# Kernel optimization log

Hardware: AMD Instinct MI355X
Metric: run time of the kernel (lower is better)

Reference implementation:

```python
import jax, jax.numpy as jnp
import numpy as np

N = 100000   # nodes
E = 500000   # edges per relation
R = 3        # relations (etypes)
L = 2        # layers
F = 300      # input features
H = 256      # hidden
C = 23       # classes


def setup_inputs() -> dict:
    key = jax.random.key(0)
    ks = jax.random.split(key, 12)
    s = 0.05
    return {
        "x": jax.random.normal(ks[0], (N, F), jnp.float32),
        "edge_src": jax.random.randint(ks[1], (R, E), 0, N, dtype=jnp.int32),
        "edge_dst": jax.random.randint(ks[2], (R, E), 0, N, dtype=jnp.int32),
        "W_feat": jax.random.normal(ks[3], (F, H), jnp.float32) * s,
        "b_feat": jnp.zeros((H,), jnp.float32),
        "g_feat": jnp.ones((H,), jnp.float32),
        "beta_feat": jnp.zeros((H,), jnp.float32),
        "gcn_W": jax.random.normal(ks[4], (L, R, H, H), jnp.float32) * s,
        "gcn_b": jnp.zeros((L, R, H), jnp.float32),
        "skip_W": jax.random.normal(ks[5], (L, H, H), jnp.float32) * s,
        "skip_b": jnp.zeros((L, H), jnp.float32),
        "bn_g": jnp.ones((L, H), jnp.float32),
        "bn_b": jnp.zeros((L, H), jnp.float32),
        "W_c1": jax.random.normal(ks[6], (H, H), jnp.float32) * s,
        "b_c1": jnp.zeros((H,), jnp.float32),
        "g_c": jnp.ones((H,), jnp.float32),
        "beta_c": jnp.zeros((H,), jnp.float32),
        "W_c2": jax.random.normal(ks[7], (H, C), jnp.float32) * s,
        "b_c2": jnp.zeros((C,), jnp.float32),
    }


def _bn(h, g, b):
    # BatchNorm1d, training-mode batch stats (biased var), eps=1e-5
    m = h.mean(0)
    v = jnp.mean((h - m) ** 2, 0)
    return g * (h - m) * jax.lax.rsqrt(v + 1e-5) + b


def _het_forward(x, edge_src, edge_dst, W_feat, b_feat, g_feat, beta_feat,
                 gcn_W, gcn_b, skip_W, skip_b, bn_g, bn_b,
                 W_c1, b_c1, g_c, beta_c, W_c2, b_c2):
    seg = jax.ops.segment_sum
    ones = jnp.ones((E,), jnp.float32)
    # feat_reduce: Linear + BN + ReLU
    h = jax.nn.relu(_bn(x @ W_feat + b_feat, g_feat, beta_feat))  # [N, H]
    for l in range(L):
        h_res = h @ skip_W[l] + skip_b[l]
        rel = []
        for r in range(R):  # per-relation GraphConv (DGL norm='both')
            src, dst = edge_src[r], edge_dst[r]
            dout = jnp.clip(seg(ones, src, num_segments=N), 1.0, None)
            din = jnp.clip(seg(ones, dst, num_segments=N), 1.0, None)
            xs = h * jax.lax.rsqrt(dout)[:, None]          # src-normalize
            m = seg(xs[src], dst, num_segments=N)          # gather-scatter
            m = m * jax.lax.rsqrt(din)[:, None]            # dst-normalize
            rel.append(m @ gcn_W[l, r] + gcn_b[l, r])
        h = jnp.mean(jnp.stack(rel, 0), 0)  # het_combine='mean'
        h = h + h_res
        h = jax.nn.leaky_relu(_bn(h, bn_g[l], bn_b[l]), 0.01)
        # dropout is identity in eval mode
    # classification head
    h = jax.nn.relu(_bn(h @ W_c1 + b_c1, g_c, beta_c))
    return h @ W_c2 + b_c2  # [N, C]


def reference(x, edge_src, edge_dst, W_feat, b_feat, g_feat, beta_feat,
              gcn_W, gcn_b, skip_W, skip_b, bn_g, bn_b,
              W_c1, b_c1, g_c, beta_c, W_c2, b_c2):
    return _het_forward(x, edge_src, edge_dst, W_feat, b_feat, g_feat,
                        beta_feat, gcn_W, gcn_b, skip_W, skip_b, bn_g, bn_b,
                        W_c1, b_c1, g_c, beta_c, W_c2, b_c2)
```

## Files before the change

### kernel.cpp

```cpp
#include <hip/hip_runtime.h>

#define NN 100000
#define EE 500000
#define RR 3
#define LL 2
#define FF 300
#define HH 256
#define CC 23
#define MPAD 100096
#define SCHUNK 2048
#define SNB ((NN + SCHUNK - 1) / SCHUNK)

static inline int cdiv_h(int a, int b) { return (a + b - 1) / b; }

typedef __attribute__((ext_vector_type(8))) short bf16x8;
typedef __attribute__((ext_vector_type(4))) float f32x4;

__device__ inline unsigned short f2bf(float f) {
    union { float f; unsigned int u; } v; v.f = f;
    unsigned int r = v.u + 0x7fff + ((v.u >> 16) & 1);
    return (unsigned short)(r >> 16);
}
__device__ inline float bf2f(unsigned short u) {
    union { unsigned int u; float f; } v; v.u = ((unsigned int)u) << 16;
    return v.f;
}
__device__ inline void gl_lds16(const void* g, void* l) {
    __builtin_amdgcn_global_load_lds((const __attribute__((address_space(1))) unsigned int*)g,
                                     (__attribute__((address_space(3))) unsigned int*)l,
                                     16, 0, 0);
}

__global__ void hist_kernel(const int* __restrict__ src, const int* __restrict__ dst,
                            int* __restrict__ cnt_out, int* __restrict__ cnt_in,
                            int RE, int Eper) {
    int i = blockIdx.x * blockDim.x + threadIdx.x;
    if (i >= RE) return;
    int r = i / Eper;
    atomicAdd(&cnt_out[r * NN + src[i]], 1);
    atomicAdd(&cnt_in[r * NN + dst[i]], 1);
}

__global__ void rs_kernel(const int* __restrict__ cnt_out, const int* __restrict__ cnt_in,
                          float* __restrict__ rs_out, float* __restrict__ rs_in, int total) {
    int i = blockIdx.x * blockDim.x + threadIdx.x;
    if (i >= total) return;
    rs_out[i] = rsqrtf(fmaxf((float)cnt_out[i], 1.0f));
    rs_in[i]  = rsqrtf(fmaxf((float)cnt_in[i], 1.0f));
}

__global__ __launch_bounds__(256) void scan_a(const int* __restrict__ cnt, int* __restrict__ bsum) {
    int r = blockIdx.y, b = blockIdx.x, t = threadIdx.x;
    const int* c = cnt + (size_t)r * NN;
    int base = b * SCHUNK;
    int s = 0;
    for (int i = t; i < SCHUNK; i += 256) {
        int idx = base + i;
        if (idx < NN) s += c[idx];
    }
#pragma unroll
    for (int o = 1; o < 64; o <<= 1) s += __shfl_xor(s, o);
    __shared__ int sh[4];
    if ((t & 63) == 0) sh[t >> 6] = s;
    __syncthreads();
    if (t == 0) bsum[r * SNB + b] = sh[0] + sh[1] + sh[2] + sh[3];
}

__global__ void scan_b(int* __restrict__ bsum, int* __restrict__ offs) {
    int r = threadIdx.x;
    if (r >= RR) return;
    int* bs = bsum + r * SNB;
    int run = 0;
    for (int i = 0; i < SNB; i++) { int v = bs[i]; bs[i] = run; run += v; }
    offs[(size_t)r * (NN + 1) + NN] = run;
}

__global__ __launch_bounds__(256) void scan_c(const int* __restrict__ cnt, const int* __restrict__ bsum,
                                              int* __restrict__ offs, int* __restrict__ cur) {
    int r = blockIdx.y, b = blockIdx.x, t = threadIdx.x;
    const int* c = cnt + (size_t)r * NN;
    int base = b * SCHUNK + t * 8;
    int v[8]; int s = 0;
#pragma unroll
    for (int j = 0; j < 8; j++) {
        int idx = base + j;
        v[j] = (idx < NN) ? c[idx] : 0;
        s += v[j];
    }
    __shared__ int sh[256];
    sh[t] = s;
    __syncthreads();
    for (int d = 1; d < 256; d <<= 1) {
        int x = (t >= d) ? sh[t - d] : 0;
        __syncthreads();
        sh[t] += x;
        __syncthreads();
    }
    int run = sh[t] - s + bsum[r * SNB + b];
    int* orow = offs + (size_t)r * (NN + 1);
    int* crow = cur + (size_t)r * NN;
#pragma unroll
    for (int j = 0; j < 8; j++) {
        int idx = base + j;
        if (idx < NN) { orow[idx] = run; crow[idx] = run; }
        run += v[j];
    }
}

__global__ void fill_kernel(const int* __restrict__ src, const int* __restrict__ dst,
                            const float* __restrict__ rs_out,
                            int* __restrict__ cur, int2* __restrict__ srcw,
                            int RE, int Eper) {
    int i = blockIdx.x * blockDim.x + threadIdx.x;
    if (i >= RE) return;
    int r = i / Eper;
    int d = dst[i];
    int s = src[i];
    float w = rs_out[r * NN + s];
    int pos = atomicAdd(&cur[r * NN + d], 1);
    srcw[(size_t)r * Eper + pos] = make_int2(s, __float_as_int(w));
}

__global__ void convert_x(const float* __restrict__ x, unsigned short* __restrict__ xpad) {
    int row = blockIdx.x;
    int col = threadIdx.x;
    float v = (row < NN && col < FF) ? x[(size_t)row * FF + col] : 0.f;
    xpad[(size_t)row * 320 + col] = f2bf(v);
}

__global__ void wprep_feat(const float* __restrict__ W, unsigned short* __restrict__ Bt) {
    int n = blockIdx.x;
    int k = threadIdx.x;
    float v = (k < FF) ? W[(size_t)k * HH + n] : 0.f;
    Bt[(size_t)n * 320 + k] = f2bf(v);
}

__global__ void wprep_layer(const float* __restrict__ skipW, const float* __restrict__ gcnW,
                            unsigned short* __restrict__ Bt) {
    int idx = blockIdx.x * blockDim.x + threadIdx.x;
    int n = idx >> 10, k = idx & 1023;
    int seg = k >> 8, k2 = k & 255;
    float v = (seg == 0) ? skipW[(size_t)k2 * HH + n]
                         : gcnW[(size_t)(seg - 1) * HH * HH + (size_t)k2 * HH + n] * (1.0f / 3.0f);
    Bt[(size_t)n * 1024 + k] = f2bf(v);
}

__global__ void bias_layer(const float* __restrict__ skip_b, const float* __restrict__ gcn_b,
                           float* __restrict__ bias) {
    int t = threadIdx.x;
    bias[t] = skip_b[t] + (gcn_b[t] + gcn_b[HH + t] + gcn_b[2 * HH + t]) * (1.0f / 3.0f);
}

__global__ void wprep_c1(const float* __restrict__ W, unsigned short* __restrict__ Bt) {
    int idx = blockIdx.x * blockDim.x + threadIdx.x;
    int n = idx >> 8, k = idx & 255;
    Bt[(size_t)n * HH + k] = f2bf(W[(size_t)k * HH + n]);
}

__global__ void wprep_c2(const float* __restrict__ W, unsigned short* __restrict__ Bt) {
    int n = blockIdx.x;
    int k = threadIdx.x;
    float v = (n < CC) ? W[(size_t)k * CC + n] : 0.f;
    Bt[(size_t)n * HH + k] = f2bf(v);
}

__global__ __launch_bounds__(256) void agg_bf16(unsigned short* __restrict__ hcat,
                                                const int* __restrict__ offs_all,
                                                const int2* __restrict__ srcw_all,
                                                const float* __restrict__ rs_in_all) {
    int r = blockIdx.y;
    const int* offs = offs_all + (size_t)r * (NN + 1);
    const int2* srcw = srcw_all + (size_t)r * EE;
    const float* rs_i = rs_in_all + (size_t)r * NN;
    int wave = threadIdx.x >> 6;
    int lane = threadIdx.x & 63;
    int node = blockIdx.x * 4 + wave;
    if (node >= NN) return;
    int s0 = __builtin_amdgcn_readfirstlane(offs[node]);
    int s1 = __builtin_amdgcn_readfirstlane(offs[node + 1]);
    int cnt = s1 - s0;
    const int2* ew = srcw + s0;
    const unsigned short* hb = hcat + lane * 4;
    float a0 = 0.f, a1 = 0.f, a2 = 0.f, a3 = 0.f;
    int k = 0;
    for (; k + 8 <= cnt; k += 8) {
        int2 e[8];
#pragma unroll
        for (int q = 0; q < 8; q++) e[q] = ew[k + q];
        ushort4 hv[8];
#pragma unroll
        for (int q = 0; q < 8; q++) hv[q] = *(const ushort4*)(hb + (size_t)e[q].x * 1024);
#pragma unroll
        for (int q = 0; q < 8; q++) {
            float u = __int_as_float(e[q].y);
            a0 += u * bf2f(hv[q].x); a1 += u * bf2f(hv[q].y);
            a2 += u * bf2f(hv[q].z); a3 += u * bf2f(hv[q].w);
        }
    }
    if (k + 4 <= cnt) {
        int2 e[4];
#pragma unroll
        for (int q = 0; q < 4; q++) e[q] = ew[k + q];
        ushort4 hv[4];
#pragma unroll
        for (int q = 0; q < 4; q++) hv[q] = *(const ushort4*)(hb + (size_t)e[q].x * 1024);
#pragma unroll
        for (int q = 0; q < 4; q++) {
            float u = __int_as_float(e[q].y);
            a0 += u * bf2f(hv[q].x); a1 += u * bf2f(hv[q].y);
            a2 += u * bf2f(hv[q].z); a3 += u * bf2f(hv[q].w);
        }
        k += 4;
    }
    int rem = cnt - k;
    if (rem > 0) {
        int2 e[3];
#pragma unroll
        for (int q = 0; q < 3; q++) {
            int kk = k + q; if (kk > cnt - 1) kk = cnt - 1;
            e[q] = ew[kk];
        }
        ushort4 hv[3];
#pragma unroll
        for (int q = 0; q < 3; q++) hv[q] = *(const ushort4*)(hb + (size_t)e[q].x * 1024);
        float u0 = __int_as_float(e[0].y);
        float u1 = rem > 1 ? __int_as_float(e[1].y) : 0.f;
        float u2 = rem > 2 ? __int_as_float(e[2].y) : 0.f;
        a0 += u0 * bf2f(hv[0].x) + u1 * bf2f(hv[1].x) + u2 * bf2f(hv[2].x);
        a1 += u0 * bf2f(hv[0].y) + u1 * bf2f(hv[1].y) + u2 * bf2f(hv[2].y);
        a2 += u0 * bf2f(hv[0].z) + u1 * bf2f(hv[1].z) + u2 * bf2f(hv[2].z);
        a3 += u0 * bf2f(hv[0].w) + u1 * bf2f(hv[1].w) + u2 * bf2f(hv[2].w);
    }
    float wi = rs_i[node];
    ushort4 o;
    o.x = f2bf(a0 * wi); o.y = f2bf(a1 * wi);
    o.z = f2bf(a2 * wi); o.w = f2bf(a3 * wi);
    *(ushort4*)(hcat + (size_t)node * 1024 + 256 * (r + 1) + lane * 4) = o;
}

__global__ __launch_bounds__(256) void mfma_gemm(const unsigned short* __restrict__ A, int ldA,
                                                 const unsigned short* __restrict__ Bt,
                                                 const float* __restrict__ bias,
                                                 void* __restrict__ Cv, int ldC,
                                                 int Nstore, int K, int c_bf16,
                                                 float* __restrict__ stats) {
    __shared__ unsigned short ldsA[2][128 * 32];
    __shared__ unsigned short ldsB[2][128 * 32];
    int tid = threadIdx.x;
    int w = tid >> 6, lane = tid & 63;
    int quad = lane >> 4, lr = lane & 15;
    int bm = blockIdx.y * 128, bn = blockIdx.x * 128;
    int wm = w >> 1, wn = w & 1;
    int lrow = lane >> 2;
    int lslot = lane & 3;

    f32x4 acc[4][4];
#pragma unroll
    for (int i = 0; i < 4; i++)
#pragma unroll
        for (int j = 0; j < 4; j++) acc[i][j] = (f32x4){0.f, 0.f, 0.f, 0.f};

    for (int k0 = 0; k0 < K; k0 += 64) {
#pragma unroll
        for (int h = 0; h < 2; h++) {
            int kk0 = k0 + h * 32;
#pragma unroll
            for (int c = 0; c < 2; c++) {
                int cc = w * 2 + c;
                int rA = cc * 16 + lrow;
                int cg = lslot ^ ((rA >> 1) & 3);
                gl_lds16(A + (size_t)(bm + rA) * ldA + kk0 + cg * 8, &ldsA[h][cc * 512]);
                gl_lds16(Bt + (size_t)(bn + rA) * K + kk0 + cg * 8, &ldsB[h][cc * 512]);
            }
        }
        __syncthreads();
#pragma unroll
        for (int h = 0; h < 2; h++) {
            bf16x8 af[4], bfr[4];
#pragma unroll
            for (int i = 0; i < 4; i++) {
                int r = wm * 64 + i * 16 + lr;
                int s = quad ^ ((r >> 1) & 3);
                af[i] = *(const bf16x8*)&ldsA[h][r * 32 + s * 8];
            }
#pragma unroll
            for (int j = 0; j < 4; j++) {
                int n = wn * 64 + j * 16 + lr;
                int s = quad ^ ((n >> 1) & 3);
                bfr[j] = *(const bf16x8*)&ldsB[h][n * 32 + s * 8];
            }
#pragma unroll
            for (int i = 0; i < 4; i++)
#pragma unroll
                for (int j = 0; j < 4; j++)
                    acc[i][j] = __builtin_amdgcn_mfma_f32_16x16x32_bf16(af[i], bfr[j], acc[i][j], 0, 0, 0);
        }
        __syncthreads();
    }

    float* Cf = (float*)Cv;
    unsigned short* Cb = (unsigned short*)Cv;
#pragma unroll
    for (int j = 0; j < 4; j++) {
        int col = bn + wn * 64 + j * 16 + lr;
        if (col >= Nstore) continue;
        float bv = bias ? bias[col] : 0.f;
        float ssum = 0.f, ssq = 0.f;
#pragma unroll
        for (int i = 0; i < 4; i++) {
#pragma unroll
            for (int v = 0; v < 4; v++) {
                int row = bm + wm * 64 + i * 16 + quad * 4 + v;
                if (row < NN) {
                    float val = acc[i][j][v] + bv;
                    if (c_bf16) Cb[(size_t)row * ldC + col] = f2bf(val);
                    else        Cf[(size_t)row * ldC + col] = val;
                    ssum += val; ssq += val * val;
                }
            }
        }
        if (stats) {
            ssum += __shfl_xor(ssum, 16); ssum += __shfl_xor(ssum, 32);
            ssq  += __shfl_xor(ssq, 16);  ssq  += __shfl_xor(ssq, 32);
            if (quad == 0) {
                atomicAdd(&stats[col], ssum);
                atomicAdd(&stats[HH + col], ssq);
            }
        }
    }
}

__global__ void bn_coef(const float* __restrict__ stats, const float* __restrict__ g,
                        const float* __restrict__ b, float* __restrict__ coef, float invM) {
    int c = threadIdx.x;
    float mean = stats[c] * invM;
    float var = stats[HH + c] * invM - mean * mean;
    float inv = rsqrtf(var + 1e-5f);
    float sc = g[c] * inv;
    coef[c] = sc;
    coef[HH + c] = b[c] - mean * sc;
}

__global__ __launch_bounds__(256) void bn_apply_v(const unsigned short* __restrict__ Z,
                                                  const float* __restrict__ coef,
                                                  unsigned short* __restrict__ out, int act) {
    int idx = blockIdx.x * blockDim.x + threadIdx.x;
    if (idx >= NN * 32) return;
    int row = idx >> 5, cg = (idx & 31) * 8;
    union { uint4 u; unsigned short s[8]; } zin, zo;
    zin.u = *(const uint4*)(Z + (size_t)row * HH + cg);
    f32x4 sc0 = *(const f32x4*)(coef + cg);
    f32x4 sc1 = *(const f32x4*)(coef + cg + 4);
    f32x4 sh0 = *(const f32x4*)(coef + HH + cg);
    f32x4 sh1 = *(const f32x4*)(coef + HH + cg + 4);
#pragma unroll
    for (int j = 0; j < 8; j++) {
        float sc = (j < 4) ? sc0[j] : sc1[j - 4];
        float sh = (j < 4) ? sh0[j] : sh1[j - 4];
        float v = bf2f(zin.s[j]) * sc + sh;
        if (act == 1) v = fmaxf(v, 0.f);
        else v = (v < 0.f) ? 0.01f * v : v;
        zo.s[j] = f2bf(v);
    }
    *(uint4*)(out + (size_t)row * 1024 + cg) = zo.u;
}

extern "C" void kernel_launch(void* const* d_in, const int* in_sizes, int n_in,
                              void* d_out, int out_size, void* d_ws, size_t ws_size,
                              hipStream_t stream) {
    const float* x        = (const float*)d_in[0];
    const int*   esrc     = (const int*)d_in[1];
    const int*   edst     = (const int*)d_in[2];
    const float* W_feat   = (const float*)d_in[3];
    const float* b_feat   = (const float*)d_in[4];
    const float* g_feat   = (const float*)d_in[5];
    const float* beta_feat= (const float*)d_in[6];
    const float* gcn_W    = (const float*)d_in[7];
    const float* gcn_b    = (const float*)d_in[8];
    const float* skip_W   = (const float*)d_in[9];
    const float* skip_b   = (const float*)d_in[10];
    const float* bn_g     = (const float*)d_in[11];
    const float* bn_b     = (const float*)d_in[12];
    const float* W_c1     = (const float*)d_in[13];
    const float* b_c1     = (const float*)d_in[14];
    const float* g_c      = (const float*)d_in[15];
    const float* beta_c   = (const float*)d_in[16];
    const float* W_c2     = (const float*)d_in[17];
    const float* b_c2     = (const float*)d_in[18];
    float* out = (float*)d_out;
    (void)in_sizes; (void)n_in; (void)out_size; (void)ws_size;

    char* w = (char*)d_ws;
    size_t off = 0;
    auto alloc = [&](size_t bytes) { void* p = w + off; off += (bytes + 255) & ~(size_t)255; return p; };
    unsigned short* hcat = (unsigned short*)alloc((size_t)MPAD * 1024 * 2);
    unsigned short* xpad = hcat;
    unsigned short* c_acc = (unsigned short*)alloc((size_t)NN * HH * 2);
    float* f_stats = (float*)alloc(4 * 2 * HH * 4);
    float* f_coef  = (float*)alloc(2 * HH * 4);
    float* f_rs_out = (float*)alloc((size_t)RR * NN * 4);
    float* f_rs_in  = (float*)alloc((size_t)RR * NN * 4);
    int* i_cnt_out = (int*)alloc((size_t)RR * NN * 4);
    int* i_cnt_in  = (int*)alloc((size_t)RR * NN * 4);
    int* i_off     = (int*)alloc((size_t)RR * (NN + 1) * 4);
    int* i_cur     = (int*)alloc((size_t)RR * NN * 4);
    int2* i_srcw   = (int2*)alloc((size_t)RR * EE * 8);
    int* i_bsum    = (int*)alloc((size_t)RR * SNB * 4);
    unsigned short* Bt_feat = (unsigned short*)alloc(256 * 320 * 2);
    unsigned short* Bt_l0   = (unsigned short*)alloc(256 * 1024 * 2);
    unsigned short* Bt_l1   = (unsigned short*)alloc(256 * 1024 * 2);
    unsigned short* Bt_c1   = (unsigned short*)alloc(256 * 256 * 2);
    unsigned short* Bt_c2   = (unsigned short*)alloc(128 * 256 * 2);
    float* bias_l0 = (float*)alloc(HH * 4);
    float* bias_l1 = (float*)alloc(HH * 4);

    const float invM = 1.0f / (float)NN;
    const int RE = RR * EE;

    (void)hipMemsetAsync(i_cnt_out, 0, (size_t)RR * NN * 4, stream);
    (void)hipMemsetAsync(i_cnt_in, 0, (size_t)RR * NN * 4, stream);
    (void)hipMemsetAsync(f_stats, 0, 4 * 2 * HH * 4, stream);
    hist_kernel<<<cdiv_h(RE, 256), 256, 0, stream>>>(esrc, edst, i_cnt_out, i_cnt_in, RE, EE);
    rs_kernel<<<cdiv_h(RR * NN, 256), 256, 0, stream>>>(i_cnt_out, i_cnt_in, f_rs_out, f_rs_in, RR * NN);
    scan_a<<<dim3(SNB, RR), 256, 0, stream>>>(i_cnt_in, i_bsum);
    scan_b<<<1, 64, 0, stream>>>(i_bsum, i_off);
    scan_c<<<dim3(SNB, RR), 256, 0, stream>>>(i_cnt_in, i_bsum, i_off, i_cur);
    fill_kernel<<<cdiv_h(RE, 256), 256, 0, stream>>>(esrc, edst, f_rs_out, i_cur, i_srcw, RE, EE);

    convert_x<<<MPAD, 320, 0, stream>>>(x, xpad);
    wprep_feat<<<256, 320, 0, stream>>>(W_feat, Bt_feat);
    wprep_layer<<<1024, 256, 0, stream>>>(skip_W, gcn_W, Bt_l0);
    wprep_layer<<<1024, 256, 0, stream>>>(skip_W + (size_t)HH * HH, gcn_W + (size_t)RR * HH * HH, Bt_l1);
    bias_layer<<<1, 256, 0, stream>>>(skip_b, gcn_b, bias_l0);
    bias_layer<<<1, 256, 0, stream>>>(skip_b + HH, gcn_b + (size_t)RR * HH, bias_l1);
    wprep_c1<<<256, 256, 0, stream>>>(W_c1, Bt_c1);
    wprep_c2<<<128, 256, 0, stream>>>(W_c2, Bt_c2);

    dim3 grid_H(2, MPAD / 128);
    dim3 grid_C(1, MPAD / 128);
    const int nblk_a = cdiv_h(NN * 32, 256);
    float* st0 = f_stats;
    float* st1 = f_stats + 2 * HH;
    float* st2 = f_stats + 4 * HH;
    float* st3 = f_stats + 6 * HH;

    mfma_gemm<<<grid_H, 256, 0, stream>>>(xpad, 320, Bt_feat, b_feat, c_acc, HH, HH, 320, 1, st0);
    bn_coef<<<1, 256, 0, stream>>>(st0, g_feat, beta_feat, f_coef, invM);
    bn_apply_v<<<nblk_a, 256, 0, stream>>>(c_acc, f_coef, hcat, 1);

    for (int l = 0; l < LL; l++) {
        agg_bf16<<<dim3(cdiv_h(NN, 4), RR), 256, 0, stream>>>(hcat, i_off, i_srcw, f_rs_in);
        float* st = l ? st2 : st1;
        mfma_gemm<<<grid_H, 256, 0, stream>>>(hcat, 1024, l ? Bt_l1 : Bt_l0,
                                              l ? bias_l1 : bias_l0, c_acc, HH, HH, 1024, 1, st);
        bn_coef<<<1, 256, 0, stream>>>(st, bn_g + (size_t)l * HH, bn_b + (size_t)l * HH, f_coef, invM);
        bn_apply_v<<<nblk_a, 256, 0, stream>>>(c_acc, f_coef, hcat, 2);
    }

    mfma_gemm<<<grid_H, 256, 0, stream>>>(hcat, 1024, Bt_c1, b_c1, c_acc, HH, HH, 256, 1, st3);
    bn_coef<<<1, 256, 0, stream>>>(st3, g_c, beta_c, f_coef, invM);
    bn_apply_v<<<nblk_a, 256, 0, stream>>>(c_acc, f_coef, hcat + 256, 1);
    mfma_gemm<<<grid_C, 256, 0, stream>>>(hcat + 256, 1024, Bt_c2, b_c2, out, CC, CC, 256, 0, nullptr);
}
```

Baseline: 1.233 ms.

## Widen GEMM tile to full N, merge weight-prep and BN-coef launches

The GEMM now uses a 128x256 tile per block covering all 256 output columns, so each A tile is read once rather than twice, with launch bounds set to 2 waves per SIMD. The seven weight-prep and bias kernels become a single launch, and BN coefficient computation moves into each bn_apply block through shared memory, dropping separate one-block launches. The wider tile doubles accumulators and B LDS, which may cut occupancy. The final 23-column GEMM now computes a full 256-wide tile with padded Bt_c2, adding wasted work there.

```diff
diff --git a/kernel.cpp b/kernel.cpp
--- a/kernel.cpp
+++ b/kernel.cpp
@@ -128,40 +128,44 @@
     xpad[(size_t)row * 320 + col] = f2bf(v);
 }
 
-__global__ void wprep_feat(const float* __restrict__ W, unsigned short* __restrict__ Bt) {
-    int n = blockIdx.x;
-    int k = threadIdx.x;
-    float v = (k < FF) ? W[(size_t)k * HH + n] : 0.f;
-    Bt[(size_t)n * 320 + k] = f2bf(v);
-}
-
-__global__ void wprep_layer(const float* __restrict__ skipW, const float* __restrict__ gcnW,
-                            unsigned short* __restrict__ Bt) {
-    int idx = blockIdx.x * blockDim.x + threadIdx.x;
-    int n = idx >> 10, k = idx & 1023;
-    int seg = k >> 8, k2 = k & 255;
-    float v = (seg == 0) ? skipW[(size_t)k2 * HH + n]
-                         : gcnW[(size_t)(seg - 1) * HH * HH + (size_t)k2 * HH + n] * (1.0f / 3.0f);
-    Bt[(size_t)n * 1024 + k] = f2bf(v);
-}
-
-__global__ void bias_layer(const float* __restrict__ skip_b, const float* __restrict__ gcn_b,
-                           float* __restrict__ bias) {
-    int t = threadIdx.x;
-    bias[t] = skip_b[t] + (gcn_b[t] + gcn_b[HH + t] + gcn_b[2 * HH + t]) * (1.0f / 3.0f);
-}
-
-__global__ void wprep_c1(const float* __restrict__ W, unsigned short* __restrict__ Bt) {
-    int idx = blockIdx.x * blockDim.x + threadIdx.x;
-    int n = idx >> 8, k = idx & 255;
-    Bt[(size_t)n * HH + k] = f2bf(W[(size_t)k * HH + n]);
-}
-
-__global__ void wprep_c2(const float* __restrict__ W, unsigned short* __restrict__ Bt) {
-    int n = blockIdx.x;
-    int k = threadIdx.x;
-    float v = (n < CC) ? W[(size_t)k * CC + n] : 0.f;
-    Bt[(size_t)n * HH + k] = f2bf(v);
+__global__ void prep_weights(const float* __restrict__ W_feat,
+                             const float* __restrict__ skip_W, const float* __restrict__ gcn_W,
+                             const float* __restrict__ skip_b, const float* __restrict__ gcn_b,
+                             const float* __restrict__ W_c1, const float* __restrict__ W_c2,
+                             unsigned short* __restrict__ Bt_feat,
+                             unsigned short* __restrict__ Bt_l0, unsigned short* __restrict__ Bt_l1,
+                             unsigned short* __restrict__ Bt_c1, unsigned short* __restrict__ Bt_c2,
+                             float* __restrict__ bias_l0, float* __restrict__ bias_l1) {
+    int b = blockIdx.x, t = threadIdx.x;
+    if (b < 256) {
+        for (int k = t; k < 320; k += 256) {
+            float v = (k < FF) ? W_feat[(size_t)k * HH + b] : 0.f;
+            Bt_feat[(size_t)b * 320 + k] = f2bf(v);
+        }
+    } else if (b < 2304) {
+        int l = (b < 1280) ? 0 : 1;
+        unsigned short* Bt = l ? Bt_l1 : Bt_l0;
+        const float* sW = skip_W + (size_t)l * HH * HH;
+        const float* gW = gcn_W + (size_t)l * RR * HH * HH;
+        int idx = (b - (l ? 1280 : 256)) * 256 + t;
+        int n = idx >> 10, k = idx & 1023;
+        int seg = k >> 8, k2 = k & 255;
+        float v = (seg == 0) ? sW[(size_t)k2 * HH + n]
+                             : gW[(size_t)(seg - 1) * HH * HH + (size_t)k2 * HH + n] * (1.0f / 3.0f);
+        Bt[(size_t)n * 1024 + k] = f2bf(v);
+    } else if (b < 2560) {
+        int idx = (b - 2304) * 256 + t;
+        int n = idx >> 8, k = idx & 255;
+        Bt_c1[(size_t)n * HH + k] = f2bf(W_c1[(size_t)k * HH + n]);
+    } else if (b < 2816) {
+        int n = b - 2560, k = t;
+        float v = (n < CC) ? W_c2[(size_t)k * CC + n] : 0.f;
+        Bt_c2[(size_t)n * HH + k] = f2bf(v);
+    } else {
+        bias_l0[t] = skip_b[t] + (gcn_b[t] + gcn_b[HH + t] + gcn_b[2 * HH + t]) * (1.0f / 3.0f);
+        bias_l1[t] = skip_b[HH + t] +
+                     (gcn_b[RR * HH + t] + gcn_b[(RR + 1) * HH + t] + gcn_b[(RR + 2) * HH + t]) * (1.0f / 3.0f);
+    }
 }
 
 __global__ __launch_bounds__(256) void agg_bf16(unsigned short* __restrict__ hcat,
@@ -238,25 +242,24 @@
     *(ushort4*)(hcat + (size_t)node * 1024 + 256 * (r + 1) + lane * 4) = o;
 }
 
-__global__ __launch_bounds__(256) void mfma_gemm(const unsigned short* __restrict__ A, int ldA,
-                                                 const unsigned short* __restrict__ Bt,
-                                                 const float* __restrict__ bias,
-                                                 void* __restrict__ Cv, int ldC,
-                                                 int Nstore, int K, int c_bf16,
-                                                 float* __restrict__ stats) {
+__global__ __launch_bounds__(256, 2) void mfma_gemm(const unsigned short* __restrict__ A, int ldA,
+                                                    const unsigned short* __restrict__ Bt,
+                                                    const float* __restrict__ bias,
+                                                    void* __restrict__ Cv, int ldC,
+                                                    int Nstore, int K, int c_bf16,
+                                                    float* __restrict__ stats) {
     __shared__ unsigned short ldsA[2][128 * 32];
-    __shared__ unsigned short ldsB[2][128 * 32];
+    __shared__ unsigned short ldsB[2][256 * 32];
     int tid = threadIdx.x;
     int w = tid >> 6, lane = tid & 63;
     int quad = lane >> 4, lr = lane & 15;
-    int bm = blockIdx.y * 128, bn = blockIdx.x * 128;
-    int wm = w >> 1, wn = w & 1;
+    int bm = blockIdx.x * 128;
     int lrow = lane >> 2;
     int lslot = lane & 3;
 
-    f32x4 acc[4][4];
-#pragma unroll
-    for (int i = 0; i < 4; i++)
+    f32x4 acc[8][4];
+#pragma unroll
+    for (int i = 0; i < 8; i++)
 #pragma unroll
         for (int j = 0; j < 4; j++) acc[i][j] = (f32x4){0.f, 0.f, 0.f, 0.f};
 
@@ -270,27 +273,33 @@
                 int rA = cc * 16 + lrow;
                 int cg = lslot ^ ((rA >> 1) & 3);
                 gl_lds16(A + (size_t)(bm + rA) * ldA + kk0 + cg * 8, &ldsA[h][cc * 512]);
-                gl_lds16(Bt + (size_t)(bn + rA) * K + kk0 + cg * 8, &ldsB[h][cc * 512]);
+            }
+#pragma unroll
+            for (int c = 0; c < 4; c++) {
+                int cc = w * 4 + c;
+                int rB = cc * 16 + lrow;
+                int cg = lslot ^ ((rB >> 1) & 3);
+                gl_lds16(Bt + (size_t)rB * K + kk0 + cg * 8, &ldsB[h][cc * 512]);
             }
         }
         __syncthreads();
 #pragma unroll
         for (int h = 0; h < 2; h++) {
-            bf16x8 af[4], bfr[4];
-#pragma unroll
-            for (int i = 0; i < 4; i++) {
-                int r = wm * 64 + i * 16 + lr;
+            bf16x8 af[8], bfr[4];
+#pragma unroll
+            for (int i = 0; i < 8; i++) {
+                int r = i * 16 + lr;
                 int s = quad ^ ((r >> 1) & 3);
                 af[i] = *(const bf16x8*)&ldsA[h][r * 32 + s * 8];
             }
 #pragma unroll
             for (int j = 0; j < 4; j++) {
-                int n = wn * 64 + j * 16 + lr;
+                int n = w * 64 + j * 16 + lr;
                 int s = quad ^ ((n >> 1) & 3);
                 bfr[j] = *(const bf16x8*)&ldsB[h][n * 32 + s * 8];
             }
 #pragma unroll
-            for (int i = 0; i < 4; i++)
+            for (int i = 0; i < 8; i++)
 #pragma unroll
                 for (int j = 0; j < 4; j++)
                     acc[i][j] = __builtin_amdgcn_mfma_f32_16x16x32_bf16(af[i], bfr[j], acc[i][j], 0, 0, 0);
@@ -302,15 +311,15 @@
     unsigned short* Cb = (unsigned short*)Cv;
 #pragma unroll
     for (int j = 0; j < 4; j++) {
-        int col = bn + wn * 64 + j * 16 + lr;
+        int col = w * 64 + j * 16 + lr;
         if (col >= Nstore) continue;
         float bv = bias ? bias[col] : 0.f;
         float ssum = 0.f, ssq = 0.f;
 #pragma unroll
-        for (int i = 0; i < 4; i++) {
+        for (int i = 0; i < 8; i++) {
 #pragma unroll
             for (int v = 0; v < 4; v++) {
-                int row = bm + wm * 64 + i * 16 + quad * 4 + v;
+                int row = bm + i * 16 + quad * 4 + v;
                 if (row < NN) {
                     float val = acc[i][j][v] + bv;
                     if (c_bf16) Cb[(size_t)row * ldC + col] = f2bf(val);
@@ -330,34 +339,30 @@
     }
 }
 
-__global__ void bn_coef(const float* __restrict__ stats, const float* __restrict__ g,
-                        const float* __restrict__ b, float* __restrict__ coef, float invM) {
-    int c = threadIdx.x;
-    float mean = stats[c] * invM;
-    float var = stats[HH + c] * invM - mean * mean;
-    float inv = rsqrtf(var + 1e-5f);
-    float sc = g[c] * inv;
-    coef[c] = sc;
-    coef[HH + c] = b[c] - mean * sc;
-}
-
 __global__ __launch_bounds__(256) void bn_apply_v(const unsigned short* __restrict__ Z,
-                                                  const float* __restrict__ coef,
+                                                  const float* __restrict__ stats,
+                                                  const float* __restrict__ g,
+                                                  const float* __restrict__ b,
                                                   unsigned short* __restrict__ out, int act) {
-    int idx = blockIdx.x * blockDim.x + threadIdx.x;
+    __shared__ float sc_s[HH], sh_s[HH];
+    int t = threadIdx.x;
+    {
+        float mean = stats[t] * (1.0f / NN);
+        float var = stats[HH + t] * (1.0f / NN) - mean * mean;
+        float inv = rsqrtf(var + 1e-5f);
+        float sc = g[t] * inv;
+        sc_s[t] = sc;
+        sh_s[t] = b[t] - mean * sc;
+    }
+    __syncthreads();
+    int idx = blockIdx.x * 256 + t;
     if (idx >= NN * 32) return;
     int row = idx >> 5, cg = (idx & 31) * 8;
     union { uint4 u; unsigned short s[8]; } zin, zo;
     zin.u = *(const uint4*)(Z + (size_t)row * HH + cg);
-    f32x4 sc0 = *(const f32x4*)(coef + cg);
-    f32x4 sc1 = *(const f32x4*)(coef + cg + 4);
-    f32x4 sh0 = *(const f32x4*)(coef + HH + cg);
-    f32x4 sh1 = *(const f32x4*)(coef + HH + cg + 4);
 #pragma unroll
     for (int j = 0; j < 8; j++) {
-        float sc = (j < 4) ? sc0[j] : sc1[j - 4];
-        float sh = (j < 4) ? sh0[j] : sh1[j - 4];
-        float v = bf2f(zin.s[j]) * sc + sh;
+        float v = bf2f(zin.s[j]) * sc_s[cg + j] + sh_s[cg + j];
         if (act == 1) v = fmaxf(v, 0.f);
         else v = (v < 0.f) ? 0.01f * v : v;
         zo.s[j] = f2bf(v);
@@ -397,7 +402,6 @@
     unsigned short* xpad = hcat;
     unsigned short* c_acc = (unsigned short*)alloc((size_t)NN * HH * 2);
     float* f_stats = (float*)alloc(4 * 2 * HH * 4);
-    float* f_coef  = (float*)alloc(2 * HH * 4);
     float* f_rs_out = (float*)alloc((size_t)RR * NN * 4);
     float* f_rs_in  = (float*)alloc((size_t)RR * NN * 4);
     int* i_cnt_out = (int*)alloc((size_t)RR * NN * 4);
@@ -410,11 +414,10 @@
     unsigned short* Bt_l0   = (unsigned short*)alloc(256 * 1024 * 2);
     unsigned short* Bt_l1   = (unsigned short*)alloc(256 * 1024 * 2);
     unsigned short* Bt_c1   = (unsigned short*)alloc(256 * 256 * 2);
-    unsigned short* Bt_c2   = (unsigned short*)alloc(128 * 256 * 2);
+    unsigned short* Bt_c2   = (unsigned short*)alloc(256 * 256 * 2);
     float* bias_l0 = (float*)alloc(HH * 4);
     float* bias_l1 = (float*)alloc(HH * 4);
 
-    const float invM = 1.0f / (float)NN;
     const int RE = RR * EE;
 
     (void)hipMemsetAsync(i_cnt_out, 0, (size_t)RR * NN * 4, stream);
@@ -428,37 +431,29 @@
     fill_kernel<<<cdiv_h(RE, 256), 256, 0, stream>>>(esrc, edst, f_rs_out, i_cur, i_srcw, RE, EE);
 
     convert_x<<<MPAD, 320, 0, stream>>>(x, xpad);
-    wprep_feat<<<256, 320, 0, stream>>>(W_feat, Bt_feat);
-    wprep_layer<<<1024, 256, 0, stream>>>(skip_W, gcn_W, Bt_l0);
-    wprep_layer<<<1024, 256, 0, stream>>>(skip_W + (size_t)HH * HH, gcn_W + (size_t)RR * HH * HH, Bt_l1);
-    bias_layer<<<1, 256, 0, stream>>>(skip_b, gcn_b, bias_l0);
-    bias_layer<<<1, 256, 0, stream>>>(skip_b + HH, gcn_b + (size_t)RR * HH, bias_l1);
-    wprep_c1<<<256, 256, 0, stream>>>(W_c1, Bt_c1);
-    wprep_c2<<<128, 256, 0, stream>>>(W_c2, Bt_c2);
-
-    dim3 grid_H(2, MPAD / 128);
-    dim3 grid_C(1, MPAD / 128);
-    const int nblk_a = cdiv_h(NN * 32, 256);
+    prep_weights<<<2817, 256, 0, stream>>>(W_feat, skip_W, gcn_W, skip_b, gcn_b, W_c1, W_c2,
+                                           Bt_feat, Bt_l0, Bt_l1, Bt_c1, Bt_c2, bias_l0, bias_l1);
+
+    const int grid_M = MPAD / 128;
+    const int nblk_a = NN * 32 / 256;
     float* st0 = f_stats;
     float* st1 = f_stats + 2 * HH;
     float* st2 = f_stats + 4 * HH;
     float* st3 = f_stats + 6 * HH;
 
-    mfma_gemm<<<grid_H, 256, 0, stream>>>(xpad, 320, Bt_feat, b_feat, c_acc, HH, HH, 320, 1, st0);
-    bn_coef<<<1, 256, 0, stream>>>(st0, g_feat, beta_feat, f_coef, invM);
-    bn_apply_v<<<nblk_a, 256, 0, stream>>>(c_acc, f_coef, hcat, 1);
+    mfma_gemm<<<grid_M, 256, 0, stream>>>(xpad, 320, Bt_feat, b_feat, c_acc, HH, HH, 320, 1, st0);
+    bn_apply_v<<<nblk_a, 256, 0, stream>>>(c_acc, st0, g_feat, beta_feat, hcat, 1);
 
     for (int l = 0; l < LL; l++) {
         agg_bf16<<<dim3(cdiv_h(NN, 4), RR), 256, 0, stream>>>(hcat, i_off, i_srcw, f_rs_in);
         float* st = l ? st2 : st1;
-        mfma_gemm<<<grid_H, 256, 0, stream>>>(hcat, 1024, l ? Bt_l1 : Bt_l0,
+        mfma_gemm<<<grid_M, 256, 0, stream>>>(hcat, 1024, l ? Bt_l1 : Bt_l0,
                                               l ? bias_l1 : bias_l0, c_acc, HH, HH, 1024, 1, st);
-        bn_coef<<<1, 256, 0, stream>>>(st, bn_g + (size_t)l * HH, bn_b + (size_t)l * HH, f_coef, invM);
-        bn_apply_v<<<nblk_a, 256, 0, stream>>>(c_acc, f_coef, hcat, 2);
-    }
-
-    mfma_gemm<<<grid_H, 256, 0, stream>>>(hcat, 1024, Bt_c1, b_c1, c_acc, HH, HH, 256, 1, st3);
-    bn_coef<<<1, 256, 0, stream>>>(st3, g_c, beta_c, f_coef, invM);
-    bn_apply_v<<<nblk_a, 256, 0, stream>>>(c_acc, f_coef, hcat + 256, 1);
-    mfma_gemm<<<grid_C, 256, 0, stream>>>(hcat + 256, 1024, Bt_c2, b_c2, out, CC, CC, 256, 0, nullptr);
-}
+        bn_apply_v<<<nblk_a, 256, 0, stream>>>(c_acc, st, bn_g + (size_t)l * HH,
+                                               bn_b + (size_t)l * HH, hcat, 2);
+    }
+
+    mfma_gemm<<<grid_M, 256, 0, stream>>>(hcat, 1024, Bt_c1, b_c1, c_acc, HH, HH, 256, 1, st3);
+    bn_apply_v<<<nblk_a, 256, 0, stream>>>(c_acc, st3, g_c, beta_c, hcat + 256, 1);
+    mfma_gemm<<<grid_M, 256, 0, stream>>>(hcat + 256, 1024, Bt_c2, b_c2, out, CC, CC, 256, 0, nullptr);
+}
```

New measurement: 1.263 ms. +2.4%, slower.
